# Kernel tuning notes

Measured on AMD Instinct MI355X. Metric: run time of the kernel, lower is better.

Reference implementation:

```python
import jax, jax.numpy as jnp
import numpy as np
from jax import lax

TEMPERATURE = 0.7
EPS = 1e-12

def _l2norm(x):
    # torch F.normalize(p=2, dim=-1) with eps clamp
    n = jnp.sqrt(jnp.sum(x * x, axis=-1, keepdims=True))
    return x / jnp.maximum(n, EPS)

def setup_inputs() -> dict:
    key = jax.random.key(0)
    k1, k2, k3 = jax.random.split(key, 3)
    B, D, A = 16384, 1024, 4096
    base_raw = jax.random.normal(k1, (B, D), dtype=jnp.float32)
    W = jnp.eye(D, dtype=jnp.float32) + 0.01 * jax.random.normal(k2, (D, D), dtype=jnp.float32)
    b = jnp.zeros((D,), dtype=jnp.float32)
    atom_bank = 0.1 * jax.random.normal(k3, (A, D), dtype=jnp.float32)
    return {"base_raw": base_raw, "W": W, "b": b, "atom_bank": atom_bank, "topk": 128}

def reference(base_raw, W, b, atom_bank, topk):
    B, D = base_raw.shape
    A = atom_bank.shape[0]
    base_emb = _l2norm(base_raw)
    # _weights_from_base: normalized projection vs normalized atoms (cosine scores)
    q = _l2norm(base_raw @ W.T + b)          # [B, D]
    a = _l2norm(atom_bank)                   # [A, D]
    scores = q @ a.T                         # [B, A]
    k = max(1, int(topk))
    if k >= A:
        weights = jax.nn.softmax(scores / TEMPERATURE, axis=-1)
    else:
        topv, topi = lax.top_k(scores, k)    # [B, k]
        topw = jax.nn.softmax(topv / TEMPERATURE, axis=-1)
        rows = jnp.arange(B)[:, None]
        weights = jnp.zeros_like(scores).at[rows, topi].set(topw)  # dense scatter
    # _reconstruct
    euc_raw = weights @ atom_bank            # [B, D]
    euc_vec = _l2norm(euc_raw)
    return (base_emb, weights, scores, euc_raw, euc_vec)
```

## Files before the change

kernel.cpp:

```cpp
#include <hip/hip_runtime.h>
#include <hip/hip_bf16.h>


#define B_ROWS 16384
#define D_DIM  1024
#define A_ATOMS 4096
#define K_TOP  128

#define KC_PANEL 512

__global__ __launch_bounds__(256) void rownorm_np_kernel(const float* __restrict__ src,
                                                         float* __restrict__ dst,
                                                         int nrows) {
    const int r = blockIdx.x * 4 + (threadIdx.x >> 6);
    if (r >= nrows) return;
    const int lane = threadIdx.x & 63;
    const int leaf = lane >> 3, j = lane & 7;
    const float* p = src + (size_t)r * D_DIM + leaf * 128 + j;

    float x[16];
    x[0] = p[0];
    float rs = __fmul_rn(x[0], x[0]);
#pragma unroll
    for (int i = 1; i < 16; i++) {
        x[i] = p[i * 8];
        rs = __fadd_rn(rs, __fmul_rn(x[i], x[i]));
    }
    rs = __fadd_rn(rs, __shfl_xor(rs, 1));
    rs = __fadd_rn(rs, __shfl_xor(rs, 2));
    rs = __fadd_rn(rs, __shfl_xor(rs, 4));
    rs = __fadd_rn(rs, __shfl_xor(rs, 8));
    rs = __fadd_rn(rs, __shfl_xor(rs, 16));
    rs = __fadd_rn(rs, __shfl_xor(rs, 32));

    const float nrm = fmaxf(__fsqrt_rn(rs), 1e-12f);
    float* q = dst + (size_t)r * D_DIM + leaf * 128 + j;
#pragma unroll
    for (int i = 0; i < 16; i++) q[i * 8] = __fdiv_rn(x[i], nrm);
}

#define GT_M 128
#define GT_N 128
#define GT_K 16

__global__ __launch_bounds__(256) void gemm_pass_f32(const float* __restrict__ A,
                                                     const float* __restrict__ Bm,
                                                     const float* __restrict__ bias,
                                                     float* __restrict__ C,
                                                     int N, int Kd,
                                                     int kbeg, int kend,
                                                     int final_pass) {
    __shared__ float As[GT_K][GT_M + 4];
    __shared__ float Bs[GT_K][GT_N + 4];
    const int ntiles = N / GT_N;
    const int bn = blockIdx.x % ntiles;
    const int bm = blockIdx.x / ntiles;
    const int m0 = bm * GT_M, n0 = bn * GT_N;
    const int t = threadIdx.x;
    const int tx = t & 15, ty = t >> 4;
    const int lr = t >> 1;
    const int lk = (t & 1) * 8;

    const float* Arow = A + (size_t)(m0 + lr) * Kd + lk;
    const float* Brow = Bm + (size_t)(n0 + lr) * Kd + lk;

    float acc[8][8];
#pragma unroll
    for (int i = 0; i < 8; i++)
#pragma unroll
        for (int j = 0; j < 8; j++) acc[i][j] = 0.f;

    {
        const float4 a0 = *(const float4*)(Arow + kbeg);
        const float4 a1 = *(const float4*)(Arow + kbeg + 4);
        const float4 b0 = *(const float4*)(Brow + kbeg);
        const float4 b1 = *(const float4*)(Brow + kbeg + 4);
        As[lk + 0][lr] = a0.x; As[lk + 1][lr] = a0.y; As[lk + 2][lr] = a0.z; As[lk + 3][lr] = a0.w;
        As[lk + 4][lr] = a1.x; As[lk + 5][lr] = a1.y; As[lk + 6][lr] = a1.z; As[lk + 7][lr] = a1.w;
        Bs[lk + 0][lr] = b0.x; Bs[lk + 1][lr] = b0.y; Bs[lk + 2][lr] = b0.z; Bs[lk + 3][lr] = b0.w;
        Bs[lk + 4][lr] = b1.x; Bs[lk + 5][lr] = b1.y; Bs[lk + 6][lr] = b1.z; Bs[lk + 7][lr] = b1.w;
    }
    __syncthreads();

    for (int k0 = kbeg; k0 < kend; k0 += GT_K) {
        const bool has_next = (k0 + GT_K < kend);
        float4 na0, na1, nb0, nb1;
        if (has_next) {
            na0 = *(const float4*)(Arow + k0 + GT_K);
            na1 = *(const float4*)(Arow + k0 + GT_K + 4);
            nb0 = *(const float4*)(Brow + k0 + GT_K);
            nb1 = *(const float4*)(Brow + k0 + GT_K + 4);
        }
#pragma unroll
        for (int k = 0; k < GT_K; k++) {
            const float4 av0 = *(const float4*)&As[k][ty * 8];
            const float4 av1 = *(const float4*)&As[k][ty * 8 + 4];
            const float4 bv0 = *(const float4*)&Bs[k][tx * 4];
            const float4 bv1 = *(const float4*)&Bs[k][64 + tx * 4];
            const float af[8] = {av0.x, av0.y, av0.z, av0.w, av1.x, av1.y, av1.z, av1.w};
            const float bf[8] = {bv0.x, bv0.y, bv0.z, bv0.w, bv1.x, bv1.y, bv1.z, bv1.w};
#pragma unroll
            for (int i = 0; i < 8; i++)
#pragma unroll
                for (int j = 0; j < 8; j++)
                    acc[i][j] = __fmaf_rn(af[i], bf[j], acc[i][j]);
        }
        if (has_next) {
            __syncthreads();
            As[lk + 0][lr] = na0.x; As[lk + 1][lr] = na0.y; As[lk + 2][lr] = na0.z; As[lk + 3][lr] = na0.w;
            As[lk + 4][lr] = na1.x; As[lk + 5][lr] = na1.y; As[lk + 6][lr] = na1.z; As[lk + 7][lr] = na1.w;
            Bs[lk + 0][lr] = nb0.x; Bs[lk + 1][lr] = nb0.y; Bs[lk + 2][lr] = nb0.z; Bs[lk + 3][lr] = nb0.w;
            Bs[lk + 4][lr] = nb1.x; Bs[lk + 5][lr] = nb1.y; Bs[lk + 6][lr] = nb1.z; Bs[lk + 7][lr] = nb1.w;
            __syncthreads();
        }
    }

    if (!final_pass) {
#pragma unroll
        for (int i = 0; i < 8; i++) {
            const size_t row = (size_t)(m0 + ty * 8 + i);
            float4 c0, c1;
            c0.x = acc[i][0]; c0.y = acc[i][1]; c0.z = acc[i][2]; c0.w = acc[i][3];
            c1.x = acc[i][4]; c1.y = acc[i][5]; c1.z = acc[i][6]; c1.w = acc[i][7];
            *(float4*)(C + row * (size_t)N + n0 + tx * 4) = c0;
            *(float4*)(C + row * (size_t)N + n0 + 64 + tx * 4) = c1;
        }
    } else {
        float bj[8];
#pragma unroll
        for (int j = 0; j < 4; j++) {
            bj[j]     = bias ? bias[n0 + tx * 4 + j]      : 0.f;
            bj[4 + j] = bias ? bias[n0 + 64 + tx * 4 + j] : 0.f;
        }
#pragma unroll
        for (int i = 0; i < 8; i++) {
            const size_t row = (size_t)(m0 + ty * 8 + i);
            float* cp0 = C + row * (size_t)N + n0 + tx * 4;
            float* cp1 = C + row * (size_t)N + n0 + 64 + tx * 4;
            const float4 p0a = *(const float4*)cp0;
            const float4 p0b = *(const float4*)cp1;
            float4 c0, c1;
            c0.x = __fadd_rn(__fadd_rn(p0a.x, acc[i][0]), bj[0]);
            c0.y = __fadd_rn(__fadd_rn(p0a.y, acc[i][1]), bj[1]);
            c0.z = __fadd_rn(__fadd_rn(p0a.z, acc[i][2]), bj[2]);
            c0.w = __fadd_rn(__fadd_rn(p0a.w, acc[i][3]), bj[3]);
            c1.x = __fadd_rn(__fadd_rn(p0b.x, acc[i][4]), bj[4]);
            c1.y = __fadd_rn(__fadd_rn(p0b.y, acc[i][5]), bj[5]);
            c1.z = __fadd_rn(__fadd_rn(p0b.z, acc[i][6]), bj[6]);
            c1.w = __fadd_rn(__fadd_rn(p0b.w, acc[i][7]), bj[7]);
            *(float4*)cp0 = c0;
            *(float4*)cp1 = c1;
        }
    }
}

__device__ __forceinline__ unsigned f2key(float f) {
    unsigned u = __float_as_uint(f);
    return (u & 0x80000000u) ? ~u : (u | 0x80000000u);
}

__global__ __launch_bounds__(256) void topk32_kernel(const float* __restrict__ scores,
                                                     float* __restrict__ weights,
                                                     float* __restrict__ list) {
    __shared__ float s[A_ATOMS];
    __shared__ unsigned hist[256];
    __shared__ int scanb[256];
    __shared__ float fred[8];
    __shared__ unsigned ubc[4];
    __shared__ unsigned char selb[A_ATOMS];

    const int r = blockIdx.x;
    const int t = threadIdx.x;
    const int lane = t & 63, wid = t >> 6;
    const float* srow = scores + (size_t)r * A_ATOMS;

#pragma unroll
    for (int c = 0; c < 4; c++) {
        const int i = c * 1024 + t * 4;
        *(float4*)(s + i) = *(const float4*)(srow + i);
    }
    __syncthreads();

    unsigned prefix = 0, remaining = K_TOP;
    for (int shift = 24; shift >= 0; shift -= 8) {
        hist[t] = 0u;
        __syncthreads();
        for (int j = 0; j < 16; j++) {
            const unsigned u = f2key(s[t * 16 + j]);
            const bool isc = (shift == 24) || ((u >> (shift + 8)) == (prefix >> (shift + 8)));
            if (isc) atomicAdd(&hist[(u >> shift) & 255u], 1u);
        }
        __syncthreads();
        scanb[t] = (int)hist[t];
        __syncthreads();
        for (int off = 1; off < 256; off <<= 1) {
            const int add = (t + off < 256) ? scanb[t + off] : 0;
            __syncthreads();
            scanb[t] += add;
            __syncthreads();
        }
        const int sfx = scanb[t];
        const int sfxn = (t < 255) ? scanb[t + 1] : 0;
        if (sfx >= (int)remaining && sfxn < (int)remaining) {
            ubc[0] = prefix | ((unsigned)t << shift);
            ubc[1] = remaining - (unsigned)sfxn;
        }
        __syncthreads();
        prefix = ubc[0];
        remaining = ubc[1];
    }
    const unsigned Tkey = prefix;
    const int need = (int)remaining;

    int myeq = 0;
    for (int j = 0; j < 16; j++) {
        const int i = t * 16 + j;
        const unsigned u = f2key(s[i]);
        selb[i] = (u > Tkey) ? 1 : 0;
        myeq += (u == Tkey) ? 1 : 0;
    }
    scanb[t] = myeq;
    __syncthreads();
    for (int off = 1; off < 256; off <<= 1) {
        const int v = scanb[t];
        const int add = (t >= off) ? scanb[t - off] : 0;
        __syncthreads();
        scanb[t] = v + add;
        __syncthreads();
    }
    int epos = scanb[t] - myeq;
    for (int j = 0; j < 16; j++) {
        const int i = t * 16 + j;
        if (f2key(s[i]) == Tkey) { if (epos < need) selb[i] = 1; epos++; }
    }
    __syncthreads();

    float zmax = -3.4e38f;
    for (int j = 0; j < 16; j++) {
        const int i = t * 16 + j;
        if (selb[i]) zmax = fmaxf(zmax, __fdiv_rn(s[i], 0.7f));
    }
    for (int o = 32; o > 0; o >>= 1) zmax = fmaxf(zmax, __shfl_down(zmax, o, 64));
    if (lane == 0) fred[wid] = zmax;
    __syncthreads();
    if (t == 0) fred[4] = fmaxf(fmaxf(fred[0], fred[1]), fmaxf(fred[2], fred[3]));
    __syncthreads();
    const float zm = fred[4];

    float esum = 0.f;
    int selcnt = 0;
    for (int j = 0; j < 16; j++) {
        const int i = t * 16 + j;
        if (selb[i]) { esum += expf(__fdiv_rn(s[i], 0.7f) - zm); selcnt++; }
    }
    for (int o = 32; o > 0; o >>= 1) esum += __shfl_down(esum, o, 64);
    if (lane == 0) fred[wid] = esum;
    __syncthreads();
    if (t == 0) fred[4] = fred[0] + fred[1] + fred[2] + fred[3];
    __syncthreads();
    const float S = fred[4];

    float* wrow = weights + (size_t)r * A_ATOMS;
#pragma unroll
    for (int c = 0; c < 4; c++) {
        const int i = c * 1024 + t * 4;
        float4 w4;
        float wv[4];
#pragma unroll
        for (int j = 0; j < 4; j++) {
            wv[j] = selb[i + j]
                ? __fdiv_rn(expf(__fdiv_rn(s[i + j], 0.7f) - zm), S)
                : 0.f;
        }
        w4.x = wv[0]; w4.y = wv[1]; w4.z = wv[2]; w4.w = wv[3];
        *(float4*)(wrow + i) = w4;
    }

    __syncthreads();
    scanb[t] = selcnt;
    __syncthreads();
    for (int off = 1; off < 256; off <<= 1) {
        const int v = scanb[t];
        const int add = (t >= off) ? scanb[t - off] : 0;
        __syncthreads();
        scanb[t] = v + add;
        __syncthreads();
    }
    int pos = scanb[t] - selcnt;
    int* li = (int*)(list + (size_t)r * 256);
    float* lw = list + (size_t)r * 256 + 128;
    for (int j = 0; j < 16; j++) {
        const int i = t * 16 + j;
        if (selb[i]) {
            const float w = __fdiv_rn(expf(__fdiv_rn(s[i], 0.7f) - zm), S);
            if (pos < K_TOP) { li[pos] = i; lw[pos] = w; }
            pos++;
        }
    }
}

__global__ __launch_bounds__(256) void euc_gather_kernel(const float* __restrict__ atoms,
                                                         const float* __restrict__ list,
                                                         float* __restrict__ euc) {
    __shared__ int sidx[K_TOP];
    __shared__ float sw[K_TOP];
    const int r = blockIdx.x, t = threadIdx.x;
    if (t < K_TOP) {
        sidx[t] = ((const int*)list)[(size_t)r * 256 + t];
        sw[t] = list[(size_t)r * 256 + 128 + t];
    }
    __syncthreads();
    const float4* A4 = (const float4*)atoms;
    float4 acc = {0.f, 0.f, 0.f, 0.f};
#pragma unroll 4
    for (int j = 0; j < K_TOP; j++) {
        const float w = sw[j];
        const float4 a = A4[(size_t)sidx[j] * 256 + t];
        acc.x = __fmaf_rn(w, a.x, acc.x);
        acc.y = __fmaf_rn(w, a.y, acc.y);
        acc.z = __fmaf_rn(w, a.z, acc.z);
        acc.w = __fmaf_rn(w, a.w, acc.w);
    }
    ((float4*)euc)[(size_t)r * 256 + t] = acc;
}

extern "C" void kernel_launch(void* const* d_in, const int* in_sizes, int n_in,
                              void* d_out, int out_size, void* d_ws, size_t ws_size,
                              hipStream_t stream) {
    const float* base_raw = (const float*)d_in[0];
    const float* W        = (const float*)d_in[1];
    const float* bvec     = (const float*)d_in[2];
    const float* atoms    = (const float*)d_in[3];
    float* out = (float*)d_out;

    const size_t BD = (size_t)B_ROWS * D_DIM;
    const size_t BA = (size_t)B_ROWS * A_ATOMS;
    float* base_emb = out;
    float* weights  = out + BD;
    float* scores   = out + BD + BA;
    float* euc_raw  = out + BD + 2 * BA;
    float* euc_vec  = out + 2 * BD + 2 * BA;

    float* a_norm = base_emb;
    float* q      = weights;
    float* list   = euc_vec;

    const int grid_q = (B_ROWS / GT_M) * (D_DIM / GT_N);
    const int grid_s = (B_ROWS / GT_M) * (A_ATOMS / GT_N);

    rownorm_np_kernel<<<A_ATOMS / 4, 256, 0, stream>>>(atoms, a_norm, A_ATOMS);
    gemm_pass_f32<<<grid_q, 256, 0, stream>>>(base_raw, W, nullptr, q,
                                              D_DIM, D_DIM, 0, KC_PANEL, 0);
    gemm_pass_f32<<<grid_q, 256, 0, stream>>>(base_raw, W, bvec, q,
                                              D_DIM, D_DIM, KC_PANEL, D_DIM, 1);
    rownorm_np_kernel<<<B_ROWS / 4, 256, 0, stream>>>(q, q, B_ROWS);
    gemm_pass_f32<<<grid_s, 256, 0, stream>>>(q, a_norm, nullptr, scores,
                                              A_ATOMS, D_DIM, 0, KC_PANEL, 0);
    gemm_pass_f32<<<grid_s, 256, 0, stream>>>(q, a_norm, nullptr, scores,
                                              A_ATOMS, D_DIM, KC_PANEL, D_DIM, 1);
    topk32_kernel<<<B_ROWS, 256, 0, stream>>>(scores, weights, list);
    euc_gather_kernel<<<B_ROWS, 256, 0, stream>>>(atoms, list, euc_raw);
    rownorm_np_kernel<<<B_ROWS / 4, 256, 0, stream>>>(euc_raw, euc_vec, B_ROWS);
    rownorm_np_kernel<<<B_ROWS / 4, 256, 0, stream>>>(base_raw, base_emb, B_ROWS);
}
```

Baseline: 3.228 ms.

## Widen GEMM tile with double-buffered LDS; register-resident radix top-k with wave scans

The FP32 GEMM tile grows from 128x128 to 128x256, with 8x16 accumulators per thread and double-buffered shared memory, which removes one barrier per k-step. This raises arithmetic intensity and cuts global loads per FLOP. In exchange it increases register pressure and LDS use, which may hurt occupancy. The top-k kernel now keeps keys in registers instead of shared memory, uses per-wave histograms to reduce atomic contention, replaces the LDS Hillis-Steele scans with wavefront shuffle scans, and tracks selection with bitmasks. This also changes the weights row layout to contiguous 16 elements per thread. The grid computation for the GEMM must be updated by the host to match the wider tile.

```diff
diff --git a/kernel.cpp b/kernel.cpp
--- a/kernel.cpp
+++ b/kernel.cpp
@@ -40,7 +40,7 @@
 }
 
 #define GT_M 128
-#define GT_N 128
+#define GT_N 256
 #define GT_K 16
 
 __global__ __launch_bounds__(256) void gemm_pass_f32(const float* __restrict__ A,
@@ -50,68 +50,85 @@
                                                      int N, int Kd,
                                                      int kbeg, int kend,
                                                      int final_pass) {
-    __shared__ float As[GT_K][GT_M + 4];
-    __shared__ float Bs[GT_K][GT_N + 4];
+    __shared__ float As[2][GT_K][GT_M + 4];
+    __shared__ float Bs[2][GT_K][GT_N + 4];
     const int ntiles = N / GT_N;
     const int bn = blockIdx.x % ntiles;
     const int bm = blockIdx.x / ntiles;
     const int m0 = bm * GT_M, n0 = bn * GT_N;
     const int t = threadIdx.x;
     const int tx = t & 15, ty = t >> 4;
-    const int lr = t >> 1;
-    const int lk = (t & 1) * 8;
-
-    const float* Arow = A + (size_t)(m0 + lr) * Kd + lk;
-    const float* Brow = Bm + (size_t)(n0 + lr) * Kd + lk;
-
-    float acc[8][8];
+    const int lrA = t >> 1;
+    const int lkA = (t & 1) * 8;
+
+    const float* Arow = A + (size_t)(m0 + lrA) * Kd + lkA;
+    const float* Brow = Bm + (size_t)(n0 + t) * Kd;
+
+    float acc[8][16];
 #pragma unroll
     for (int i = 0; i < 8; i++)
 #pragma unroll
-        for (int j = 0; j < 8; j++) acc[i][j] = 0.f;
+        for (int j = 0; j < 16; j++) acc[i][j] = 0.f;
 
     {
         const float4 a0 = *(const float4*)(Arow + kbeg);
         const float4 a1 = *(const float4*)(Arow + kbeg + 4);
         const float4 b0 = *(const float4*)(Brow + kbeg);
         const float4 b1 = *(const float4*)(Brow + kbeg + 4);
-        As[lk + 0][lr] = a0.x; As[lk + 1][lr] = a0.y; As[lk + 2][lr] = a0.z; As[lk + 3][lr] = a0.w;
-        As[lk + 4][lr] = a1.x; As[lk + 5][lr] = a1.y; As[lk + 6][lr] = a1.z; As[lk + 7][lr] = a1.w;
-        Bs[lk + 0][lr] = b0.x; Bs[lk + 1][lr] = b0.y; Bs[lk + 2][lr] = b0.z; Bs[lk + 3][lr] = b0.w;
-        Bs[lk + 4][lr] = b1.x; Bs[lk + 5][lr] = b1.y; Bs[lk + 6][lr] = b1.z; Bs[lk + 7][lr] = b1.w;
-    }
-    __syncthreads();
-
+        const float4 b2 = *(const float4*)(Brow + kbeg + 8);
+        const float4 b3 = *(const float4*)(Brow + kbeg + 12);
+        As[0][lkA + 0][lrA] = a0.x; As[0][lkA + 1][lrA] = a0.y;
+        As[0][lkA + 2][lrA] = a0.z; As[0][lkA + 3][lrA] = a0.w;
+        As[0][lkA + 4][lrA] = a1.x; As[0][lkA + 5][lrA] = a1.y;
+        As[0][lkA + 6][lrA] = a1.z; As[0][lkA + 7][lrA] = a1.w;
+        Bs[0][0][t] = b0.x;  Bs[0][1][t] = b0.y;  Bs[0][2][t] = b0.z;  Bs[0][3][t] = b0.w;
+        Bs[0][4][t] = b1.x;  Bs[0][5][t] = b1.y;  Bs[0][6][t] = b1.z;  Bs[0][7][t] = b1.w;
+        Bs[0][8][t] = b2.x;  Bs[0][9][t] = b2.y;  Bs[0][10][t] = b2.z; Bs[0][11][t] = b2.w;
+        Bs[0][12][t] = b3.x; Bs[0][13][t] = b3.y; Bs[0][14][t] = b3.z; Bs[0][15][t] = b3.w;
+    }
+    __syncthreads();
+
+    int cur = 0;
     for (int k0 = kbeg; k0 < kend; k0 += GT_K) {
         const bool has_next = (k0 + GT_K < kend);
-        float4 na0, na1, nb0, nb1;
+        float4 na0, na1, nb0, nb1, nb2, nb3;
         if (has_next) {
             na0 = *(const float4*)(Arow + k0 + GT_K);
             na1 = *(const float4*)(Arow + k0 + GT_K + 4);
             nb0 = *(const float4*)(Brow + k0 + GT_K);
             nb1 = *(const float4*)(Brow + k0 + GT_K + 4);
+            nb2 = *(const float4*)(Brow + k0 + GT_K + 8);
+            nb3 = *(const float4*)(Brow + k0 + GT_K + 12);
         }
 #pragma unroll
         for (int k = 0; k < GT_K; k++) {
-            const float4 av0 = *(const float4*)&As[k][ty * 8];
-            const float4 av1 = *(const float4*)&As[k][ty * 8 + 4];
-            const float4 bv0 = *(const float4*)&Bs[k][tx * 4];
-            const float4 bv1 = *(const float4*)&Bs[k][64 + tx * 4];
+            const float4 av0 = *(const float4*)&As[cur][k][ty * 8];
+            const float4 av1 = *(const float4*)&As[cur][k][ty * 8 + 4];
+            const float4 bq0 = *(const float4*)&Bs[cur][k][tx * 4];
+            const float4 bq1 = *(const float4*)&Bs[cur][k][64 + tx * 4];
+            const float4 bq2 = *(const float4*)&Bs[cur][k][128 + tx * 4];
+            const float4 bq3 = *(const float4*)&Bs[cur][k][192 + tx * 4];
             const float af[8] = {av0.x, av0.y, av0.z, av0.w, av1.x, av1.y, av1.z, av1.w};
-            const float bf[8] = {bv0.x, bv0.y, bv0.z, bv0.w, bv1.x, bv1.y, bv1.z, bv1.w};
+            const float bf[16] = {bq0.x, bq0.y, bq0.z, bq0.w, bq1.x, bq1.y, bq1.z, bq1.w,
+                                  bq2.x, bq2.y, bq2.z, bq2.w, bq3.x, bq3.y, bq3.z, bq3.w};
 #pragma unroll
             for (int i = 0; i < 8; i++)
 #pragma unroll
-                for (int j = 0; j < 8; j++)
+                for (int j = 0; j < 16; j++)
                     acc[i][j] = __fmaf_rn(af[i], bf[j], acc[i][j]);
         }
         if (has_next) {
+            const int nxt = cur ^ 1;
+            As[nxt][lkA + 0][lrA] = na0.x; As[nxt][lkA + 1][lrA] = na0.y;
+            As[nxt][lkA + 2][lrA] = na0.z; As[nxt][lkA + 3][lrA] = na0.w;
+            As[nxt][lkA + 4][lrA] = na1.x; As[nxt][lkA + 5][lrA] = na1.y;
+            As[nxt][lkA + 6][lrA] = na1.z; As[nxt][lkA + 7][lrA] = na1.w;
+            Bs[nxt][0][t] = nb0.x;  Bs[nxt][1][t] = nb0.y;  Bs[nxt][2][t] = nb0.z;  Bs[nxt][3][t] = nb0.w;
+            Bs[nxt][4][t] = nb1.x;  Bs[nxt][5][t] = nb1.y;  Bs[nxt][6][t] = nb1.z;  Bs[nxt][7][t] = nb1.w;
+            Bs[nxt][8][t] = nb2.x;  Bs[nxt][9][t] = nb2.y;  Bs[nxt][10][t] = nb2.z; Bs[nxt][11][t] = nb2.w;
+            Bs[nxt][12][t] = nb3.x; Bs[nxt][13][t] = nb3.y; Bs[nxt][14][t] = nb3.z; Bs[nxt][15][t] = nb3.w;
             __syncthreads();
-            As[lk + 0][lr] = na0.x; As[lk + 1][lr] = na0.y; As[lk + 2][lr] = na0.z; As[lk + 3][lr] = na0.w;
-            As[lk + 4][lr] = na1.x; As[lk + 5][lr] = na1.y; As[lk + 6][lr] = na1.z; As[lk + 7][lr] = na1.w;
-            Bs[lk + 0][lr] = nb0.x; Bs[lk + 1][lr] = nb0.y; Bs[lk + 2][lr] = nb0.z; Bs[lk + 3][lr] = nb0.w;
-            Bs[lk + 4][lr] = nb1.x; Bs[lk + 5][lr] = nb1.y; Bs[lk + 6][lr] = nb1.z; Bs[lk + 7][lr] = nb1.w;
-            __syncthreads();
+            cur = nxt;
         }
     }
 
@@ -119,37 +136,35 @@
 #pragma unroll
         for (int i = 0; i < 8; i++) {
             const size_t row = (size_t)(m0 + ty * 8 + i);
-            float4 c0, c1;
-            c0.x = acc[i][0]; c0.y = acc[i][1]; c0.z = acc[i][2]; c0.w = acc[i][3];
-            c1.x = acc[i][4]; c1.y = acc[i][5]; c1.z = acc[i][6]; c1.w = acc[i][7];
-            *(float4*)(C + row * (size_t)N + n0 + tx * 4) = c0;
-            *(float4*)(C + row * (size_t)N + n0 + 64 + tx * 4) = c1;
+#pragma unroll
+            for (int g = 0; g < 4; g++) {
+                float4 c4;
+                c4.x = acc[i][g * 4 + 0]; c4.y = acc[i][g * 4 + 1];
+                c4.z = acc[i][g * 4 + 2]; c4.w = acc[i][g * 4 + 3];
+                *(float4*)(C + row * (size_t)N + n0 + g * 64 + tx * 4) = c4;
+            }
         }
     } else {
-        float bj[8];
-#pragma unroll
-        for (int j = 0; j < 4; j++) {
-            bj[j]     = bias ? bias[n0 + tx * 4 + j]      : 0.f;
-            bj[4 + j] = bias ? bias[n0 + 64 + tx * 4 + j] : 0.f;
-        }
+        float bj[16];
+#pragma unroll
+        for (int g = 0; g < 4; g++)
+#pragma unroll
+            for (int j = 0; j < 4; j++)
+                bj[g * 4 + j] = bias ? bias[n0 + g * 64 + tx * 4 + j] : 0.f;
 #pragma unroll
         for (int i = 0; i < 8; i++) {
             const size_t row = (size_t)(m0 + ty * 8 + i);
-            float* cp0 = C + row * (size_t)N + n0 + tx * 4;
-            float* cp1 = C + row * (size_t)N + n0 + 64 + tx * 4;
-            const float4 p0a = *(const float4*)cp0;
-            const float4 p0b = *(const float4*)cp1;
-            float4 c0, c1;
-            c0.x = __fadd_rn(__fadd_rn(p0a.x, acc[i][0]), bj[0]);
-            c0.y = __fadd_rn(__fadd_rn(p0a.y, acc[i][1]), bj[1]);
-            c0.z = __fadd_rn(__fadd_rn(p0a.z, acc[i][2]), bj[2]);
-            c0.w = __fadd_rn(__fadd_rn(p0a.w, acc[i][3]), bj[3]);
-            c1.x = __fadd_rn(__fadd_rn(p0b.x, acc[i][4]), bj[4]);
-            c1.y = __fadd_rn(__fadd_rn(p0b.y, acc[i][5]), bj[5]);
-            c1.z = __fadd_rn(__fadd_rn(p0b.z, acc[i][6]), bj[6]);
-            c1.w = __fadd_rn(__fadd_rn(p0b.w, acc[i][7]), bj[7]);
-            *(float4*)cp0 = c0;
-            *(float4*)cp1 = c1;
+#pragma unroll
+            for (int g = 0; g < 4; g++) {
+                float* cp = C + row * (size_t)N + n0 + g * 64 + tx * 4;
+                const float4 p0 = *(const float4*)cp;
+                float4 c4;
+                c4.x = __fadd_rn(__fadd_rn(p0.x, acc[i][g * 4 + 0]), bj[g * 4 + 0]);
+                c4.y = __fadd_rn(__fadd_rn(p0.y, acc[i][g * 4 + 1]), bj[g * 4 + 1]);
+                c4.z = __fadd_rn(__fadd_rn(p0.z, acc[i][g * 4 + 2]), bj[g * 4 + 2]);
+                c4.w = __fadd_rn(__fadd_rn(p0.w, acc[i][g * 4 + 3]), bj[g * 4 + 3]);
+                *(float4*)cp = c4;
+            }
         }
     }
 }
@@ -158,49 +173,59 @@
     unsigned u = __float_as_uint(f);
     return (u & 0x80000000u) ? ~u : (u | 0x80000000u);
 }
+__device__ __forceinline__ float key2f(unsigned k) {
+    unsigned u = (k & 0x80000000u) ? (k & 0x7fffffffu) : ~k;
+    return __uint_as_float(u);
+}
 
 __global__ __launch_bounds__(256) void topk32_kernel(const float* __restrict__ scores,
                                                      float* __restrict__ weights,
                                                      float* __restrict__ list) {
-    __shared__ float s[A_ATOMS];
-    __shared__ unsigned hist[256];
-    __shared__ int scanb[256];
+    __shared__ unsigned hist[4][256];
+    __shared__ int wtot[4];
+    __shared__ int wpre[4];
+    __shared__ unsigned ubc[2];
     __shared__ float fred[8];
-    __shared__ unsigned ubc[4];
-    __shared__ unsigned char selb[A_ATOMS];
 
     const int r = blockIdx.x;
     const int t = threadIdx.x;
     const int lane = t & 63, wid = t >> 6;
-    const float* srow = scores + (size_t)r * A_ATOMS;
-
+    const float* srow = scores + (size_t)r * A_ATOMS + (size_t)t * 16;
+
+    unsigned key[16];
 #pragma unroll
     for (int c = 0; c < 4; c++) {
-        const int i = c * 1024 + t * 4;
-        *(float4*)(s + i) = *(const float4*)(srow + i);
-    }
-    __syncthreads();
+        const float4 f = ((const float4*)srow)[c];
+        key[c * 4 + 0] = f2key(f.x); key[c * 4 + 1] = f2key(f.y);
+        key[c * 4 + 2] = f2key(f.z); key[c * 4 + 3] = f2key(f.w);
+    }
 
     unsigned prefix = 0, remaining = K_TOP;
     for (int shift = 24; shift >= 0; shift -= 8) {
-        hist[t] = 0u;
+#pragma unroll
+        for (int w = 0; w < 4; w++) hist[w][t] = 0u;
         __syncthreads();
+#pragma unroll
         for (int j = 0; j < 16; j++) {
-            const unsigned u = f2key(s[t * 16 + j]);
+            const unsigned u = key[j];
             const bool isc = (shift == 24) || ((u >> (shift + 8)) == (prefix >> (shift + 8)));
-            if (isc) atomicAdd(&hist[(u >> shift) & 255u], 1u);
+            if (isc) atomicAdd(&hist[wid][(u >> shift) & 255u], 1u);
         }
         __syncthreads();
-        scanb[t] = (int)hist[t];
+        const int c = (int)(hist[0][t] + hist[1][t] + hist[2][t] + hist[3][t]);
+        int sfx = c;
+#pragma unroll
+        for (int off = 1; off < 64; off <<= 1) {
+            const int tv = __shfl_down(sfx, off, 64);
+            sfx += (lane + off < 64) ? tv : 0;
+        }
+        if (lane == 0) wtot[wid] = sfx;
         __syncthreads();
-        for (int off = 1; off < 256; off <<= 1) {
-            const int add = (t + off < 256) ? scanb[t + off] : 0;
-            __syncthreads();
-            scanb[t] += add;
-            __syncthreads();
-        }
-        const int sfx = scanb[t];
-        const int sfxn = (t < 255) ? scanb[t + 1] : 0;
+        int addw = 0;
+#pragma unroll
+        for (int w = 0; w < 4; w++) if (w > wid) addw += wtot[w];
+        sfx += addw;
+        const int sfxn = sfx - c;
         if (sfx >= (int)remaining && sfxn < (int)remaining) {
             ubc[0] = prefix | ((unsigned)t << shift);
             ubc[1] = remaining - (unsigned)sfxn;
@@ -212,34 +237,33 @@
     const unsigned Tkey = prefix;
     const int need = (int)remaining;
 
-    int myeq = 0;
+    int selmask = 0, myeq = 0;
+#pragma unroll
     for (int j = 0; j < 16; j++) {
-        const int i = t * 16 + j;
-        const unsigned u = f2key(s[i]);
-        selb[i] = (u > Tkey) ? 1 : 0;
-        myeq += (u == Tkey) ? 1 : 0;
-    }
-    scanb[t] = myeq;
-    __syncthreads();
-    for (int off = 1; off < 256; off <<= 1) {
-        const int v = scanb[t];
-        const int add = (t >= off) ? scanb[t - off] : 0;
-        __syncthreads();
-        scanb[t] = v + add;
-        __syncthreads();
-    }
-    int epos = scanb[t] - myeq;
+        if (key[j] > Tkey) selmask |= (1 << j);
+        else if (key[j] == Tkey) myeq++;
+    }
+    int pre = myeq;
+#pragma unroll
+    for (int off = 1; off < 64; off <<= 1) {
+        const int tv = __shfl_up(pre, off, 64);
+        pre += (lane >= off) ? tv : 0;
+    }
+    if (lane == 63) wpre[wid] = pre;
+    __syncthreads();
+    int basew = 0;
+#pragma unroll
+    for (int w = 0; w < 4; w++) if (w < wid) basew += wpre[w];
+    int epos = basew + pre - myeq;
+#pragma unroll
     for (int j = 0; j < 16; j++) {
-        const int i = t * 16 + j;
-        if (f2key(s[i]) == Tkey) { if (epos < need) selb[i] = 1; epos++; }
-    }
-    __syncthreads();
+        if (key[j] == Tkey) { if (epos < need) selmask |= (1 << j); epos++; }
+    }
 
     float zmax = -3.4e38f;
-    for (int j = 0; j < 16; j++) {
-        const int i = t * 16 + j;
-        if (selb[i]) zmax = fmaxf(zmax, __fdiv_rn(s[i], 0.7f));
-    }
+#pragma unroll
+    for (int j = 0; j < 16; j++)
+        if (selmask & (1 << j)) zmax = fmaxf(zmax, __fdiv_rn(key2f(key[j]), 0.7f));
     for (int o = 32; o > 0; o >>= 1) zmax = fmaxf(zmax, __shfl_down(zmax, o, 64));
     if (lane == 0) fred[wid] = zmax;
     __syncthreads();
@@ -248,11 +272,9 @@
     const float zm = fred[4];
 
     float esum = 0.f;
-    int selcnt = 0;
-    for (int j = 0; j < 16; j++) {
-        const int i = t * 16 + j;
-        if (selb[i]) { esum += expf(__fdiv_rn(s[i], 0.7f) - zm); selcnt++; }
-    }
+#pragma unroll
+    for (int j = 0; j < 16; j++)
+        if (selmask & (1 << j)) esum += expf(__fdiv_rn(key2f(key[j]), 0.7f) - zm);
     for (int o = 32; o > 0; o >>= 1) esum += __shfl_down(esum, o, 64);
     if (lane == 0) fred[wid] = esum;
     __syncthreads();
@@ -260,40 +282,43 @@
     __syncthreads();
     const float S = fred[4];
 
-    float* wrow = weights + (size_t)r * A_ATOMS;
+    float* wrow = weights + (size_t)r * A_ATOMS + (size_t)t * 16;
 #pragma unroll
     for (int c = 0; c < 4; c++) {
-        const int i = c * 1024 + t * 4;
         float4 w4;
         float wv[4];
 #pragma unroll
         for (int j = 0; j < 4; j++) {
-            wv[j] = selb[i + j]
-                ? __fdiv_rn(expf(__fdiv_rn(s[i + j], 0.7f) - zm), S)
+            const int jj = c * 4 + j;
+            wv[j] = (selmask & (1 << jj))
+                ? __fdiv_rn(expf(__fdiv_rn(key2f(key[jj]), 0.7f) - zm), S)
                 : 0.f;
         }
         w4.x = wv[0]; w4.y = wv[1]; w4.z = wv[2]; w4.w = wv[3];
-        *(float4*)(wrow + i) = w4;
-    }
-
-    __syncthreads();
-    scanb[t] = selcnt;
-    __syncthreads();
-    for (int off = 1; off < 256; off <<= 1) {
-        const int v = scanb[t];
-        const int add = (t >= off) ? scanb[t - off] : 0;
-        __syncthreads();
-        scanb[t] = v + add;
-        __syncthreads();
-    }
-    int pos = scanb[t] - selcnt;
+        ((float4*)wrow)[c] = w4;
+    }
+
+    const int selcnt = __popc((unsigned)selmask);
+    __syncthreads();
+    int pre2 = selcnt;
+#pragma unroll
+    for (int off = 1; off < 64; off <<= 1) {
+        const int tv = __shfl_up(pre2, off, 64);
+        pre2 += (lane >= off) ? tv : 0;
+    }
+    if (lane == 63) wpre[wid] = pre2;
+    __syncthreads();
+    int basec = 0;
+#pragma unroll
+    for (int w = 0; w < 4; w++) if (w < wid) basec += wpre[w];
+    int pos = basec + pre2 - selcnt;
     int* li = (int*)(list + (size_t)r * 256);
     float* lw = list + (size_t)r * 256 + 128;
+#pragma unroll
     for (int j = 0; j < 16; j++) {
-        const int i = t * 16 + j;
-        if (selb[i]) {
-            const float w = __fdiv_rn(expf(__fdiv_rn(s[i], 0.7f) - zm), S);
-            if (pos < K_TOP) { li[pos] = i; lw[pos] = w; }
+        if (selmask & (1 << j)) {
+            const float w = __fdiv_rn(expf(__fdiv_rn(key2f(key[j]), 0.7f) - zm), S);
+            if (pos < K_TOP) { li[pos] = t * 16 + j; lw[pos] = w; }
             pos++;
         }
     }
```

New measurement: 3.120 ms. 1.03x faster.
